# Performance work log

Hardware: AMD Instinct MI355X
Metric: run time of the kernel (lower is better)

The kernel has to match this reference:

```python
import jax, jax.numpy as jnp
import numpy as np

B, T, D, O, E = 4, 4096, 256, 256, 16


def setup_inputs() -> dict:
    key = jax.random.key(0)
    ks = jax.random.split(key, 5)
    s_in = 1.0 / np.sqrt(D)
    x = jax.random.normal(ks[0], (B, T, D), dtype=jnp.float32)
    We = jax.random.uniform(ks[1], (E, D, O), minval=-s_in, maxval=s_in, dtype=jnp.float32)
    be = jax.random.uniform(ks[2], (E, O), minval=-s_in, maxval=s_in, dtype=jnp.float32)
    Wg = jax.random.uniform(ks[3], (D, E), minval=-s_in, maxval=s_in, dtype=jnp.float32)
    bg = jax.random.uniform(ks[4], (E,), minval=-s_in, maxval=s_in, dtype=jnp.float32)
    return {"x": x, "We": We, "be": be, "Wg": Wg, "bg": bg}


def reference(x, We, be, Wg, bg):
    # gate: softmax over experts  [B,T,E]
    gate = jax.nn.softmax(jnp.einsum("btd,de->bte", x, Wg) + bg, axis=-1)
    # all experts: batched GEMM  [B,T,E,O]
    h = jax.nn.gelu(jnp.einsum("btd,edo->bteo", x, We) + be, approximate=False)
    # softmax-weighted sum over experts  [B,T,O]
    return jnp.einsum("bteo,bte->bto", h, gate)
```

## Files before the change

### kernel.cpp

```cpp
#include <hip/hip_runtime.h>
#include <stdint.h>

#define KD 256
#define NO 256
#define NE 16
#define BM 64
#define BN 128
#define XROW 264
#define GROW 68

typedef short bf16x8 __attribute__((ext_vector_type(8)));
typedef float f32x4 __attribute__((ext_vector_type(4)));

__device__ __forceinline__ unsigned short f2bf(float f) {
  uint32_t u = __float_as_uint(f);
  u += 0x7fffu + ((u >> 16) & 1u);
  return (unsigned short)(u >> 16);
}
__device__ __forceinline__ float bf2f(unsigned short h) {
  return __uint_as_float(((uint32_t)h) << 16);
}
__device__ __forceinline__ float gelu_f(float h) {
#if __has_builtin(__builtin_amdgcn_exp2f)
  float zn = h * fmaf(-0.10294817f, h * h, -2.3022077f);
  return h * __builtin_amdgcn_rcpf(1.0f + __builtin_amdgcn_exp2f(zn));
#else
  float z = h * fmaf(0.07135481627f, h * h, 1.5957691216f);
  return h * __builtin_amdgcn_rcpf(1.0f + __expf(-z));
#endif
}

__global__ void moe_prep(const float* __restrict__ We, unsigned short* __restrict__ Wf,
                         const float* __restrict__ Wg, unsigned short* __restrict__ Wgt)
{
  const int tid = threadIdx.x;
  const int bid = blockIdx.x;
  const int w = tid >> 6, lane = tid & 63;
  const int g = bid * 4 + w;
  const int e = g >> 7, kc = (g >> 4) & 7, ob = g & 15;
  const int q = lane >> 4, ln = lane & 15;

  const float* src = We + ((size_t)e * KD + kc * 32 + q * 8) * NO + ob * 16 + ln;
  unsigned int pk[4];
#pragma unroll
  for (int h = 0; h < 4; ++h) {
    unsigned short lo = f2bf(src[(h * 2 + 0) * NO]);
    unsigned short hi = f2bf(src[(h * 2 + 1) * NO]);
    pk[h] = (unsigned int)lo | ((unsigned int)hi << 16);
  }
  uint4* dst = (uint4*)(Wf + ((((size_t)(e * 8 + kc) * 16 + ob) * 64) + lane) * 8);
  *dst = make_uint4(pk[0], pk[1], pk[2], pk[3]);

  if (bid == 0) {
    int d = tid;
    const float* wr = Wg + (size_t)d * NE;
#pragma unroll
    for (int ee = 0; ee < NE; ++ee)
      Wgt[ee * KD + d] = f2bf(wr[ee]);
  }
}

__launch_bounds__(256, 2)
__global__ void moe_main(const float* __restrict__ x,
                         const uint4* __restrict__ Wf,
                         const unsigned short* __restrict__ Wgt,
                         const float* __restrict__ be,
                         const float* __restrict__ bg,
                         float* __restrict__ out)
{
  __shared__ __align__(16) unsigned short Xs[BM * XROW];
  __shared__ __align__(16) float gate_t[NE * GROW];
  __shared__ unsigned short be_h[NE * BN];

  const int tid = threadIdx.x;
  const int bid = blockIdx.x;
  const int half = bid & 1;
  const int n0 = half * BN;
  const int m0 = (bid >> 1) * BM;
  const int w = tid >> 6, lane = tid & 63;
  const int ln = lane & 15, quad = lane >> 4;
  const int eoff = __builtin_amdgcn_readfirstlane(((tid >> 6) * 4 + bid) & 15);

  const int voff = (half * 8 + w * 2) * 64 + lane;

  {
    const float4* xg = (const float4*)x + (size_t)m0 * (KD / 4);
#pragma unroll
    for (int p = 0; p < 16; ++p) {
      int idx = p * 256 + tid;
      int r = idx >> 6, c = idx & 63;
      float4 v = xg[r * (KD / 4) + c];
      uint32_t lo = (uint32_t)f2bf(v.x) | ((uint32_t)f2bf(v.y) << 16);
      uint32_t hi = (uint32_t)f2bf(v.z) | ((uint32_t)f2bf(v.w) << 16);
      *(uint2*)&Xs[r * XROW + c * 4] = make_uint2(lo, hi);
    }
  }
  uint4 b[4][2];
#pragma unroll
  for (int kc = 0; kc < 4; ++kc) {
    const uint4* p = Wf + ((size_t)eoff * 8 + kc) * 1024 + voff;
    b[kc][0] = p[0]; b[kc][1] = p[64];
  }
#pragma unroll
  for (int p = 0; p < 8; ++p) {
    int idx = p * 256 + tid;
    int e = idx >> 7, c = idx & 127;
    be_h[e * BN + c] = f2bf(be[e * NO + n0 + c]);
  }
  __syncthreads();

  bf16x8 a[4][8];
#pragma unroll
  for (int i = 0; i < 4; ++i)
#pragma unroll
    for (int kc = 0; kc < 8; ++kc)
      a[i][kc] = *(const bf16x8*)&Xs[(i * 16 + ln) * XROW + kc * 32 + quad * 8];

  {
    f32x4 g = {0.f, 0.f, 0.f, 0.f};
#pragma unroll
    for (int kc = 0; kc < 8; ++kc) {
      bf16x8 af = *(const bf16x8*)&Xs[(w * 16 + ln) * XROW + kc * 32 + quad * 8];
      bf16x8 wb = *(const bf16x8*)(Wgt + (size_t)ln * KD + kc * 32 + quad * 8);
      g = __builtin_amdgcn_mfma_f32_16x16x32_bf16(af, wb, g, 0, 0, 0);
    }
    float bgl = bg[ln];
#pragma unroll
    for (int r = 0; r < 4; ++r) {
      float v = g[r] + bgl;
      float mx = v;
#pragma unroll
      for (int msk = 1; msk < 16; msk <<= 1)
        mx = fmaxf(mx, __shfl_xor(mx, msk, 64));
      float ev = __expf(v - mx);
      float s = ev;
#pragma unroll
      for (int msk = 1; msk < 16; msk <<= 1)
        s += __shfl_xor(s, msk, 64);
      gate_t[ln * GROW + w * 16 + quad * 4 + r] = ev * __builtin_amdgcn_rcpf(s);
    }
  }
  __syncthreads();

  f32x4 acc[4][2], oacc[4][2];
#pragma unroll
  for (int i = 0; i < 4; ++i)
#pragma unroll
    for (int j = 0; j < 2; ++j) {
      acc[i][j] = (f32x4){0.f, 0.f, 0.f, 0.f};
      oacc[i][j] = (f32x4){0.f, 0.f, 0.f, 0.f};
    }

#pragma unroll 1
  for (int ei = 0; ei < NE; ++ei) {
    const int e  = (eoff + ei) & 15;
    const int en = (eoff + ei + 1) & 15;
    const uint4* bse = Wf + (size_t)e  * 8192 + voff;
    const uint4* bsn = Wf + (size_t)en * 8192 + voff;

#pragma unroll
    for (int kc = 0; kc < 8; ++kc) {
      uint4* bc = b[kc & 3];
#pragma unroll
      for (int i = 0; i < 4; ++i)
#pragma unroll
        for (int j = 0; j < 2; ++j)
          acc[i][j] = __builtin_amdgcn_mfma_f32_16x16x32_bf16(
              a[i][kc], *(const bf16x8*)&bc[j], acc[i][j], 0, 0, 0);
      if (kc < 4) {
        const uint4* p = bse + (kc + 4) * 1024;
        bc[0] = p[0]; bc[1] = p[64];
      } else if (ei < NE - 1) {
        const uint4* p = bsn + (kc - 4) * 1024;
        bc[0] = p[0]; bc[1] = p[64];
      }
    }
    {
      f32x4 gv[4];
#pragma unroll
      for (int i = 0; i < 4; ++i)
        gv[i] = *(const f32x4*)&gate_t[e * GROW + i * 16 + quad * 4];
      const float bb0 = bf2f(be_h[e * BN + w * 32 + ln]);
      const float bb1 = bf2f(be_h[e * BN + w * 32 + 16 + ln]);
#pragma unroll
      for (int i = 0; i < 4; ++i)
#pragma unroll
        for (int j = 0; j < 2; ++j)
#pragma unroll
          for (int r = 0; r < 4; ++r) {
            float hh = acc[i][j][r] + (j ? bb1 : bb0);
            oacc[i][j][r] = fmaf(gv[i][r], gelu_f(hh), oacc[i][j][r]);
            acc[i][j][r] = 0.f;
          }
    }
  }

#pragma unroll
  for (int i = 0; i < 4; ++i)
#pragma unroll
    for (int r = 0; r < 4; ++r) {
      int row = m0 + i * 16 + quad * 4 + r;
      float* orow = out + (size_t)row * NO + n0 + w * 32 + ln;
      orow[0]  = oacc[i][0][r];
      orow[16] = oacc[i][1][r];
    }
}

extern "C" void kernel_launch(void* const* d_in, const int* in_sizes, int n_in,
                              void* d_out, int out_size, void* d_ws, size_t ws_size,
                              hipStream_t stream) {
  const float* x  = (const float*)d_in[0];
  const float* We = (const float*)d_in[1];
  const float* be = (const float*)d_in[2];
  const float* Wg = (const float*)d_in[3];
  const float* bg = (const float*)d_in[4];
  float* out = (float*)d_out;
  unsigned short* Wf  = (unsigned short*)d_ws;
  unsigned short* Wgt = (unsigned short*)((char*)d_ws + (size_t)NE * NO * KD * 2);

  moe_prep<<<512, 256, 0, stream>>>(We, Wf, Wg, Wgt);
  moe_main<<<512, 256, 0, stream>>>(x, (const uint4*)Wf, Wgt, be, bg, out);
}
```

Measured before the change: 120.5 us.

## Split waves into MFMA producers and GELU consumers via LDS stash

Measured after the change: 141.3 us. 17.3% more time.

```diff
diff --git a/kernel.cpp b/kernel.cpp
--- a/kernel.cpp
+++ b/kernel.cpp
@@ -60,7 +60,7 @@
   }
 }
 
-__launch_bounds__(256, 2)
+__launch_bounds__(512, 2)
 __global__ void moe_main(const float* __restrict__ x,
                          const uint4* __restrict__ Wf,
                          const unsigned short* __restrict__ Wgt,
@@ -68,7 +68,7 @@
                          const float* __restrict__ bg,
                          float* __restrict__ out)
 {
-  __shared__ __align__(16) unsigned short Xs[BM * XROW];
+  __shared__ __align__(16) unsigned short XsBuf[BM * XROW];
   __shared__ __align__(16) float gate_t[NE * GROW];
   __shared__ unsigned short be_h[NE * BN];
 
@@ -78,16 +78,20 @@
   const int n0 = half * BN;
   const int m0 = (bid >> 1) * BM;
   const int w = tid >> 6, lane = tid & 63;
+  const int wg = w & 3;
+  const bool isG = (w < 4);
   const int ln = lane & 15, quad = lane >> 4;
-  const int eoff = __builtin_amdgcn_readfirstlane(((tid >> 6) * 4 + bid) & 15);
-
-  const int voff = (half * 8 + w * 2) * 64 + lane;
+  const int eoff = __builtin_amdgcn_readfirstlane((wg * 4 + bid) & 15);
+  const int voff = (half * 8 + wg * 2) * 64 + lane;
+
+  unsigned short* const Xs = XsBuf;
+  f32x4* const stash4 = (f32x4*)XsBuf;
 
   {
     const float4* xg = (const float4*)x + (size_t)m0 * (KD / 4);
 #pragma unroll
-    for (int p = 0; p < 16; ++p) {
-      int idx = p * 256 + tid;
+    for (int p = 0; p < 8; ++p) {
+      int idx = p * 512 + tid;
       int r = idx >> 6, c = idx & 63;
       float4 v = xg[r * (KD / 4) + c];
       uint32_t lo = (uint32_t)f2bf(v.x) | ((uint32_t)f2bf(v.y) << 16);
@@ -95,32 +99,34 @@
       *(uint2*)&Xs[r * XROW + c * 4] = make_uint2(lo, hi);
     }
   }
-  uint4 b[4][2];
-#pragma unroll
-  for (int kc = 0; kc < 4; ++kc) {
-    const uint4* p = Wf + ((size_t)eoff * 8 + kc) * 1024 + voff;
-    b[kc][0] = p[0]; b[kc][1] = p[64];
-  }
-#pragma unroll
-  for (int p = 0; p < 8; ++p) {
-    int idx = p * 256 + tid;
+#pragma unroll
+  for (int p = 0; p < 4; ++p) {
+    int idx = p * 512 + tid;
     int e = idx >> 7, c = idx & 127;
     be_h[e * BN + c] = f2bf(be[e * NO + n0 + c]);
   }
+  uint4 b[4][2];
+  if (isG) {
+#pragma unroll
+    for (int kc = 0; kc < 4; ++kc) {
+      const uint4* p = Wf + ((size_t)eoff * 8 + kc) * 1024 + voff;
+      b[kc][0] = p[0]; b[kc][1] = p[64];
+    }
+  }
   __syncthreads();
 
   bf16x8 a[4][8];
-#pragma unroll
-  for (int i = 0; i < 4; ++i)
-#pragma unroll
-    for (int kc = 0; kc < 8; ++kc)
-      a[i][kc] = *(const bf16x8*)&Xs[(i * 16 + ln) * XROW + kc * 32 + quad * 8];
-
-  {
+  if (isG) {
+#pragma unroll
+    for (int i = 0; i < 4; ++i)
+#pragma unroll
+      for (int kc = 0; kc < 8; ++kc)
+        a[i][kc] = *(const bf16x8*)&Xs[(i * 16 + ln) * XROW + kc * 32 + quad * 8];
+
     f32x4 g = {0.f, 0.f, 0.f, 0.f};
 #pragma unroll
     for (int kc = 0; kc < 8; ++kc) {
-      bf16x8 af = *(const bf16x8*)&Xs[(w * 16 + ln) * XROW + kc * 32 + quad * 8];
+      bf16x8 af = *(const bf16x8*)&Xs[(wg * 16 + ln) * XROW + kc * 32 + quad * 8];
       bf16x8 wb = *(const bf16x8*)(Wgt + (size_t)ln * KD + kc * 32 + quad * 8);
       g = __builtin_amdgcn_mfma_f32_16x16x32_bf16(af, wb, g, 0, 0, 0);
     }
@@ -137,12 +143,13 @@
 #pragma unroll
       for (int msk = 1; msk < 16; msk <<= 1)
         s += __shfl_xor(s, msk, 64);
-      gate_t[ln * GROW + w * 16 + quad * 4 + r] = ev * __builtin_amdgcn_rcpf(s);
+      gate_t[ln * GROW + wg * 16 + quad * 4 + r] = ev * __builtin_amdgcn_rcpf(s);
     }
   }
   __syncthreads();
 
-  f32x4 acc[4][2], oacc[4][2];
+  f32x4 acc[4][2];
+  f32x4 oacc[4][2];
 #pragma unroll
   for (int i = 0; i < 4; ++i)
 #pragma unroll
@@ -153,57 +160,89 @@
 
 #pragma unroll 1
   for (int ei = 0; ei < NE; ++ei) {
-    const int e  = (eoff + ei) & 15;
-    const int en = (eoff + ei + 1) & 15;
-    const uint4* bse = Wf + (size_t)e  * 8192 + voff;
-    const uint4* bsn = Wf + (size_t)en * 8192 + voff;
-
-#pragma unroll
-    for (int kc = 0; kc < 8; ++kc) {
-      uint4* bc = b[kc & 3];
+    if (isG) {
+      const int e  = (eoff + ei) & 15;
+      const int en = (eoff + ei + 1) & 15;
+      const uint4* bse = Wf + (size_t)e  * 8192 + voff;
+      const uint4* bsn = Wf + (size_t)en * 8192 + voff;
+#pragma unroll
+      for (int kc = 0; kc < 8; ++kc) {
+        uint4* bc = b[kc & 3];
+#pragma unroll
+        for (int i = 0; i < 4; ++i)
+#pragma unroll
+          for (int j = 0; j < 2; ++j)
+            acc[i][j] = __builtin_amdgcn_mfma_f32_16x16x32_bf16(
+                a[i][kc], *(const bf16x8*)&bc[j], acc[i][j], 0, 0, 0);
+        if (kc < 4) {
+          const uint4* p = bse + (kc + 4) * 1024;
+          bc[0] = p[0]; bc[1] = p[64];
+        } else if (ei < NE - 1) {
+          const uint4* p = bsn + (kc - 4) * 1024;
+          bc[0] = p[0]; bc[1] = p[64];
+        }
+      }
+    } else if (ei > 0) {
+      const int ep = (eoff + ei - 1) & 15;
+      const float bb0 = bf2f(be_h[ep * BN + wg * 32 + ln]);
+      const float bb1 = bf2f(be_h[ep * BN + wg * 32 + 16 + ln]);
+#pragma unroll
+      for (int i = 0; i < 4; ++i) {
+        const f32x4 gq = *(const f32x4*)&gate_t[ep * GROW + i * 16 + quad * 4];
+#pragma unroll
+        for (int j = 0; j < 2; ++j) {
+          const f32x4 sv = stash4[(i * 2 + j) * 256 + wg * 64 + lane];
+          const float bb = j ? bb1 : bb0;
+#pragma unroll
+          for (int r = 0; r < 4; ++r) {
+            float hh = sv[r] + bb;
+            oacc[i][j][r] = fmaf(gq[r], gelu_f(hh), oacc[i][j][r]);
+          }
+        }
+      }
+    }
+    __syncthreads();
+
+    if (isG) {
 #pragma unroll
       for (int i = 0; i < 4; ++i)
 #pragma unroll
-        for (int j = 0; j < 2; ++j)
-          acc[i][j] = __builtin_amdgcn_mfma_f32_16x16x32_bf16(
-              a[i][kc], *(const bf16x8*)&bc[j], acc[i][j], 0, 0, 0);
-      if (kc < 4) {
-        const uint4* p = bse + (kc + 4) * 1024;
-        bc[0] = p[0]; bc[1] = p[64];
-      } else if (ei < NE - 1) {
-        const uint4* p = bsn + (kc - 4) * 1024;
-        bc[0] = p[0]; bc[1] = p[64];
-      }
-    }
-    {
-      f32x4 gv[4];
-#pragma unroll
-      for (int i = 0; i < 4; ++i)
-        gv[i] = *(const f32x4*)&gate_t[e * GROW + i * 16 + quad * 4];
-      const float bb0 = bf2f(be_h[e * BN + w * 32 + ln]);
-      const float bb1 = bf2f(be_h[e * BN + w * 32 + 16 + ln]);
-#pragma unroll
-      for (int i = 0; i < 4; ++i)
-#pragma unroll
-        for (int j = 0; j < 2; ++j)
-#pragma unroll
-          for (int r = 0; r < 4; ++r) {
-            float hh = acc[i][j][r] + (j ? bb1 : bb0);
-            oacc[i][j][r] = fmaf(gv[i][r], gelu_f(hh), oacc[i][j][r]);
-            acc[i][j][r] = 0.f;
-          }
-    }
-  }
-
-#pragma unroll
-  for (int i = 0; i < 4; ++i)
-#pragma unroll
-    for (int r = 0; r < 4; ++r) {
-      int row = m0 + i * 16 + quad * 4 + r;
-      float* orow = out + (size_t)row * NO + n0 + w * 32 + ln;
-      orow[0]  = oacc[i][0][r];
-      orow[16] = oacc[i][1][r];
-    }
+        for (int j = 0; j < 2; ++j) {
+          stash4[(i * 2 + j) * 256 + wg * 64 + lane] = acc[i][j];
+          acc[i][j] = (f32x4){0.f, 0.f, 0.f, 0.f};
+        }
+    }
+    __syncthreads();
+  }
+
+  if (!isG) {
+    const int ep = (eoff + NE - 1) & 15;
+    const float bb0 = bf2f(be_h[ep * BN + wg * 32 + ln]);
+    const float bb1 = bf2f(be_h[ep * BN + wg * 32 + 16 + ln]);
+#pragma unroll
+    for (int i = 0; i < 4; ++i) {
+      const f32x4 gq = *(const f32x4*)&gate_t[ep * GROW + i * 16 + quad * 4];
+#pragma unroll
+      for (int j = 0; j < 2; ++j) {
+        const f32x4 sv = stash4[(i * 2 + j) * 256 + wg * 64 + lane];
+        const float bb = j ? bb1 : bb0;
+#pragma unroll
+        for (int r = 0; r < 4; ++r) {
+          float hh = sv[r] + bb;
+          oacc[i][j][r] = fmaf(gq[r], gelu_f(hh), oacc[i][j][r]);
+        }
+      }
+    }
+#pragma unroll
+    for (int i = 0; i < 4; ++i)
+#pragma unroll
+      for (int r = 0; r < 4; ++r) {
+        int row = m0 + i * 16 + quad * 4 + r;
+        float* orow = out + (size_t)row * NO + n0 + wg * 32 + ln;
+        orow[0]  = oacc[i][0][r];
+        orow[16] = oacc[i][1][r];
+      }
+  }
 }
 
 extern "C" void kernel_launch(void* const* d_in, const int* in_sizes, int n_in,
@@ -219,5 +258,5 @@
   unsigned short* Wgt = (unsigned short*)((char*)d_ws + (size_t)NE * NO * KD * 2);
 
   moe_prep<<<512, 256, 0, stream>>>(We, Wf, Wg, Wgt);
-  moe_main<<<512, 256, 0, stream>>>(x, (const uint4*)Wf, Wgt, be, bg, out);
-}
+  moe_main<<<512, 512, 0, stream>>>(x, (const uint4*)Wf, Wgt, be, bg, out);
+}
```

## Switch expert GEMM to 32x32x16 MFMA with matching weight layout and packed epilogue

Applied to the files above, without the earlier changes.

Result: slower. 130.0 us (+7.8%).

```diff
diff --git a/kernel.cpp b/kernel.cpp
--- a/kernel.cpp
+++ b/kernel.cpp
@@ -11,6 +11,8 @@
 
 typedef short bf16x8 __attribute__((ext_vector_type(8)));
 typedef float f32x4 __attribute__((ext_vector_type(4)));
+typedef float f32x2 __attribute__((ext_vector_type(2)));
+typedef float f32x16 __attribute__((ext_vector_type(16)));
 
 __device__ __forceinline__ unsigned short f2bf(float f) {
   uint32_t u = __float_as_uint(f);
@@ -20,14 +22,20 @@
 __device__ __forceinline__ float bf2f(unsigned short h) {
   return __uint_as_float(((uint32_t)h) << 16);
 }
-__device__ __forceinline__ float gelu_f(float h) {
-#if __has_builtin(__builtin_amdgcn_exp2f)
-  float zn = h * fmaf(-0.10294817f, h * h, -2.3022077f);
-  return h * __builtin_amdgcn_rcpf(1.0f + __builtin_amdgcn_exp2f(zn));
-#else
-  float z = h * fmaf(0.07135481627f, h * h, 1.5957691216f);
-  return h * __builtin_amdgcn_rcpf(1.0f + __expf(-z));
-#endif
+__device__ __forceinline__ void epi_pair(f32x2 h, f32x2 gv, f32x2& o) {
+  f32x2 t = h * h;
+  f32x2 s = __builtin_elementwise_fma(t, (f32x2){-0.10294817f, -0.10294817f},
+                                      (f32x2){-2.3022077f, -2.3022077f});
+  f32x2 zn = h * s;
+  f32x2 ev;
+  ev.x = __builtin_amdgcn_exp2f(zn.x);
+  ev.y = __builtin_amdgcn_exp2f(zn.y);
+  f32x2 den = ev + 1.0f;
+  f32x2 r;
+  r.x = __builtin_amdgcn_rcpf(den.x);
+  r.y = __builtin_amdgcn_rcpf(den.y);
+  f32x2 g = h * r;
+  o = __builtin_elementwise_fma(gv, g, o);
 }
 
 __global__ void moe_prep(const float* __restrict__ We, unsigned short* __restrict__ Wf,
@@ -37,10 +45,10 @@
   const int bid = blockIdx.x;
   const int w = tid >> 6, lane = tid & 63;
   const int g = bid * 4 + w;
-  const int e = g >> 7, kc = (g >> 4) & 7, ob = g & 15;
-  const int q = lane >> 4, ln = lane & 15;
-
-  const float* src = We + ((size_t)e * KD + kc * 32 + q * 8) * NO + ob * 16 + ln;
+  const int e = g >> 7, kk = (g >> 3) & 15, ob2 = g & 7;
+  const int q5 = lane >> 5, c = lane & 31;
+
+  const float* src = We + ((size_t)e * KD + kk * 16 + q5 * 8) * NO + ob2 * 32 + c;
   unsigned int pk[4];
 #pragma unroll
   for (int h = 0; h < 4; ++h) {
@@ -48,7 +56,7 @@
     unsigned short hi = f2bf(src[(h * 2 + 1) * NO]);
     pk[h] = (unsigned int)lo | ((unsigned int)hi << 16);
   }
-  uint4* dst = (uint4*)(Wf + ((((size_t)(e * 8 + kc) * 16 + ob) * 64) + lane) * 8);
+  uint4* dst = (uint4*)(Wf + ((((size_t)(e * 16 + kk) * 8 + ob2) * 64) + lane) * 8);
   *dst = make_uint4(pk[0], pk[1], pk[2], pk[3]);
 
   if (bid == 0) {
@@ -79,9 +87,10 @@
   const int m0 = (bid >> 1) * BM;
   const int w = tid >> 6, lane = tid & 63;
   const int ln = lane & 15, quad = lane >> 4;
+  const int c31 = lane & 31, q5 = lane >> 5;
   const int eoff = __builtin_amdgcn_readfirstlane(((tid >> 6) * 4 + bid) & 15);
 
-  const int voff = (half * 8 + w * 2) * 64 + lane;
+  const int voff = (half * 4 + w) * 64 + lane;
 
   {
     const float4* xg = (const float4*)x + (size_t)m0 * (KD / 4);
@@ -95,12 +104,10 @@
       *(uint2*)&Xs[r * XROW + c * 4] = make_uint2(lo, hi);
     }
   }
-  uint4 b[4][2];
-#pragma unroll
-  for (int kc = 0; kc < 4; ++kc) {
-    const uint4* p = Wf + ((size_t)eoff * 8 + kc) * 1024 + voff;
-    b[kc][0] = p[0]; b[kc][1] = p[64];
-  }
+  uint4 b2[8];
+#pragma unroll
+  for (int kk = 0; kk < 8; ++kk)
+    b2[kk] = Wf[(size_t)eoff * 8192 + kk * 512 + voff];
 #pragma unroll
   for (int p = 0; p < 8; ++p) {
     int idx = p * 256 + tid;
@@ -109,12 +116,12 @@
   }
   __syncthreads();
 
-  bf16x8 a[4][8];
-#pragma unroll
-  for (int i = 0; i < 4; ++i)
-#pragma unroll
-    for (int kc = 0; kc < 8; ++kc)
-      a[i][kc] = *(const bf16x8*)&Xs[(i * 16 + ln) * XROW + kc * 32 + quad * 8];
+  bf16x8 a[2][16];
+#pragma unroll
+  for (int t = 0; t < 2; ++t)
+#pragma unroll
+    for (int kk = 0; kk < 16; ++kk)
+      a[t][kk] = *(const bf16x8*)&Xs[(t * 32 + c31) * XROW + kk * 16 + q5 * 8];
 
   {
     f32x4 g = {0.f, 0.f, 0.f, 0.f};
@@ -142,14 +149,12 @@
   }
   __syncthreads();
 
-  f32x4 acc[4][2], oacc[4][2];
-#pragma unroll
-  for (int i = 0; i < 4; ++i)
-#pragma unroll
-    for (int j = 0; j < 2; ++j) {
-      acc[i][j] = (f32x4){0.f, 0.f, 0.f, 0.f};
-      oacc[i][j] = (f32x4){0.f, 0.f, 0.f, 0.f};
-    }
+  f32x16 acc2[2], oacc2[2];
+#pragma unroll
+  for (int t = 0; t < 2; ++t) {
+#pragma unroll
+    for (int r = 0; r < 16; ++r) { acc2[t][r] = 0.f; oacc2[t][r] = 0.f; }
+  }
 
 #pragma unroll 1
   for (int ei = 0; ei < NE; ++ei) {
@@ -159,51 +164,51 @@
     const uint4* bsn = Wf + (size_t)en * 8192 + voff;
 
 #pragma unroll
-    for (int kc = 0; kc < 8; ++kc) {
-      uint4* bc = b[kc & 3];
-#pragma unroll
-      for (int i = 0; i < 4; ++i)
-#pragma unroll
-        for (int j = 0; j < 2; ++j)
-          acc[i][j] = __builtin_amdgcn_mfma_f32_16x16x32_bf16(
-              a[i][kc], *(const bf16x8*)&bc[j], acc[i][j], 0, 0, 0);
-      if (kc < 4) {
-        const uint4* p = bse + (kc + 4) * 1024;
-        bc[0] = p[0]; bc[1] = p[64];
+    for (int kk = 0; kk < 16; ++kk) {
+      const bf16x8 bw = *(const bf16x8*)&b2[kk & 7];
+#pragma unroll
+      for (int t = 0; t < 2; ++t)
+        acc2[t] = __builtin_amdgcn_mfma_f32_32x32x16_bf16(
+            a[t][kk], bw, acc2[t], 0, 0, 0);
+      if (kk < 8) {
+        b2[kk] = bse[(kk + 8) * 512];
       } else if (ei < NE - 1) {
-        const uint4* p = bsn + (kc - 4) * 1024;
-        bc[0] = p[0]; bc[1] = p[64];
+        b2[kk & 7] = bsn[(kk - 8) * 512];
       }
     }
     {
-      f32x4 gv[4];
-#pragma unroll
-      for (int i = 0; i < 4; ++i)
-        gv[i] = *(const f32x4*)&gate_t[e * GROW + i * 16 + quad * 4];
-      const float bb0 = bf2f(be_h[e * BN + w * 32 + ln]);
-      const float bb1 = bf2f(be_h[e * BN + w * 32 + 16 + ln]);
-#pragma unroll
-      for (int i = 0; i < 4; ++i)
-#pragma unroll
-        for (int j = 0; j < 2; ++j)
-#pragma unroll
-          for (int r = 0; r < 4; ++r) {
-            float hh = acc[i][j][r] + (j ? bb1 : bb0);
-            oacc[i][j][r] = fmaf(gv[i][r], gelu_f(hh), oacc[i][j][r]);
-            acc[i][j][r] = 0.f;
-          }
-    }
-  }
-
-#pragma unroll
-  for (int i = 0; i < 4; ++i)
-#pragma unroll
-    for (int r = 0; r < 4; ++r) {
-      int row = m0 + i * 16 + quad * 4 + r;
-      float* orow = out + (size_t)row * NO + n0 + w * 32 + ln;
-      orow[0]  = oacc[i][0][r];
-      orow[16] = oacc[i][1][r];
-    }
+      const float bb = bf2f(be_h[e * BN + w * 32 + c31]);
+      const f32x2 bb2 = {bb, bb};
+#pragma unroll
+      for (int t = 0; t < 2; ++t)
+#pragma unroll
+        for (int rg = 0; rg < 4; ++rg) {
+          const f32x4 gq = *(const f32x4*)&gate_t[e * GROW + t * 32 + rg * 8 + q5 * 4];
+          f32x2 h0 = {acc2[t][rg * 4 + 0], acc2[t][rg * 4 + 1]};
+          f32x2 h1 = {acc2[t][rg * 4 + 2], acc2[t][rg * 4 + 3]};
+          h0 = h0 + bb2;
+          h1 = h1 + bb2;
+          f32x2 o0 = {oacc2[t][rg * 4 + 0], oacc2[t][rg * 4 + 1]};
+          f32x2 o1 = {oacc2[t][rg * 4 + 2], oacc2[t][rg * 4 + 3]};
+          epi_pair(h0, (f32x2){gq[0], gq[1]}, o0);
+          epi_pair(h1, (f32x2){gq[2], gq[3]}, o1);
+          oacc2[t][rg * 4 + 0] = o0.x; oacc2[t][rg * 4 + 1] = o0.y;
+          oacc2[t][rg * 4 + 2] = o1.x; oacc2[t][rg * 4 + 3] = o1.y;
+          acc2[t][rg * 4 + 0] = 0.f; acc2[t][rg * 4 + 1] = 0.f;
+          acc2[t][rg * 4 + 2] = 0.f; acc2[t][rg * 4 + 3] = 0.f;
+        }
+    }
+  }
+
+#pragma unroll
+  for (int t = 0; t < 2; ++t)
+#pragma unroll
+    for (int rg = 0; rg < 4; ++rg)
+#pragma unroll
+      for (int r = 0; r < 4; ++r) {
+        int row = m0 + t * 32 + rg * 8 + q5 * 4 + r;
+        out[(size_t)row * NO + n0 + w * 32 + c31] = oacc2[t][rg * 4 + r];
+      }
 }
 
 extern "C" void kernel_launch(void* const* d_in, const int* in_sizes, int n_in,
```

## Stream expert weights into double-buffered LDS slabs via global_load_lds DMA

Applied to the files above, without the earlier changes.

Result: slower. 137.3 us (+13.9%).

```diff
diff --git a/kernel.cpp b/kernel.cpp
--- a/kernel.cpp
+++ b/kernel.cpp
@@ -28,6 +28,12 @@
   float z = h * fmaf(0.07135481627f, h * h, 1.5957691216f);
   return h * __builtin_amdgcn_rcpf(1.0f + __expf(-z));
 #endif
+}
+
+__device__ __forceinline__ void dma16(const void* g, void* l) {
+  __builtin_amdgcn_global_load_lds(
+      (const __attribute__((address_space(1))) uint32_t*)g,
+      (__attribute__((address_space(3))) uint32_t*)l, 16, 0, 0);
 }
 
 __global__ void moe_prep(const float* __restrict__ We, unsigned short* __restrict__ Wf,
@@ -60,7 +66,7 @@
   }
 }
 
-__launch_bounds__(256, 2)
+__launch_bounds__(256, 1)
 __global__ void moe_main(const float* __restrict__ x,
                          const uint4* __restrict__ Wf,
                          const unsigned short* __restrict__ Wgt,
@@ -68,9 +74,11 @@
                          const float* __restrict__ bg,
                          float* __restrict__ out)
 {
-  __shared__ __align__(16) unsigned short Xs[BM * XROW];
+  __shared__ __align__(16) unsigned char BB[131072];
   __shared__ __align__(16) float gate_t[NE * GROW];
   __shared__ unsigned short be_h[NE * BN];
+
+  unsigned short* const Xs = (unsigned short*)BB;
 
   const int tid = threadIdx.x;
   const int bid = blockIdx.x;
@@ -80,8 +88,7 @@
   const int w = tid >> 6, lane = tid & 63;
   const int ln = lane & 15, quad = lane >> 4;
   const int eoff = __builtin_amdgcn_readfirstlane(((tid >> 6) * 4 + bid) & 15);
-
-  const int voff = (half * 8 + w * 2) * 64 + lane;
+  const int obb = half * 8 + w * 2;
 
   {
     const float4* xg = (const float4*)x + (size_t)m0 * (KD / 4);
@@ -95,12 +102,6 @@
       *(uint2*)&Xs[r * XROW + c * 4] = make_uint2(lo, hi);
     }
   }
-  uint4 b[4][2];
-#pragma unroll
-  for (int kc = 0; kc < 4; ++kc) {
-    const uint4* p = Wf + ((size_t)eoff * 8 + kc) * 1024 + voff;
-    b[kc][0] = p[0]; b[kc][1] = p[64];
-  }
 #pragma unroll
   for (int p = 0; p < 8; ++p) {
     int idx = p * 256 + tid;
@@ -142,6 +143,20 @@
   }
   __syncthreads();
 
+  const char* const WfB = (const char*)Wf;
+  char* const slab0 = (char*)BB + w * 32768;
+  char* const slab1 = slab0 + 16384;
+  {
+    const char* s0 = WfB + (size_t)eoff * 131072 + (size_t)obb * 1024 + lane * 16;
+    const char* s1 = WfB + (size_t)((eoff + 1) & 15) * 131072 + (size_t)obb * 1024 + lane * 16;
+#pragma unroll
+    for (int s = 0; s < 16; ++s)
+      dma16(s0 + (s >> 1) * 16384 + (s & 1) * 1024, slab0 + s * 1024 + lane * 16);
+#pragma unroll
+    for (int s = 0; s < 16; ++s)
+      dma16(s1 + (s >> 1) * 16384 + (s & 1) * 1024, slab1 + s * 1024 + lane * 16);
+  }
+
   f32x4 acc[4][2], oacc[4][2];
 #pragma unroll
   for (int i = 0; i < 4; ++i)
@@ -153,28 +168,35 @@
 
 #pragma unroll 1
   for (int ei = 0; ei < NE; ++ei) {
-    const int e  = (eoff + ei) & 15;
-    const int en = (eoff + ei + 1) & 15;
-    const uint4* bse = Wf + (size_t)e  * 8192 + voff;
-    const uint4* bsn = Wf + (size_t)en * 8192 + voff;
-
+    const int e = (eoff + ei) & 15;
+
+    if (ei < NE - 1) {
+      asm volatile("s_waitcnt vmcnt(16)" ::: "memory");
+    } else {
+      asm volatile("s_waitcnt vmcnt(0)" ::: "memory");
+    }
+    __builtin_amdgcn_sched_barrier(0);
+
+    char* const cur = (ei & 1) ? slab1 : slab0;
 #pragma unroll
     for (int kc = 0; kc < 8; ++kc) {
-      uint4* bc = b[kc & 3];
-#pragma unroll
-      for (int i = 0; i < 4; ++i)
-#pragma unroll
-        for (int j = 0; j < 2; ++j)
-          acc[i][j] = __builtin_amdgcn_mfma_f32_16x16x32_bf16(
-              a[i][kc], *(const bf16x8*)&bc[j], acc[i][j], 0, 0, 0);
-      if (kc < 4) {
-        const uint4* p = bse + (kc + 4) * 1024;
-        bc[0] = p[0]; bc[1] = p[64];
-      } else if (ei < NE - 1) {
-        const uint4* p = bsn + (kc - 4) * 1024;
-        bc[0] = p[0]; bc[1] = p[64];
+      const bf16x8 b0 = *(const bf16x8*)(cur + (kc * 2 + 0) * 1024 + lane * 16);
+      const bf16x8 b1 = *(const bf16x8*)(cur + (kc * 2 + 1) * 1024 + lane * 16);
+#pragma unroll
+      for (int i = 0; i < 4; ++i) {
+        acc[i][0] = __builtin_amdgcn_mfma_f32_16x16x32_bf16(a[i][kc], b0, acc[i][0], 0, 0, 0);
+        acc[i][1] = __builtin_amdgcn_mfma_f32_16x16x32_bf16(a[i][kc], b1, acc[i][1], 0, 0, 0);
       }
     }
+
+    if (ei < NE - 2) {
+      const int en2 = (eoff + ei + 2) & 15;
+      const char* sn = WfB + (size_t)en2 * 131072 + (size_t)obb * 1024 + lane * 16;
+#pragma unroll
+      for (int s = 0; s < 16; ++s)
+        dma16(sn + (s >> 1) * 16384 + (s & 1) * 1024, cur + s * 1024 + lane * 16);
+    }
+
     {
       f32x4 gv[4];
 #pragma unroll
```
